# Kernel optimization log

Measured on AMD Instinct MI355X. Metric: run time of the kernel, lower is better.

Reference implementation:

```python
import jax, jax.numpy as jnp
import numpy as np
from jax import lax

B, D_MODEL, H, W = 8, 384, 64, 64
D_INNER, D_STATE, D_CONV, DT_RANK = 768, 16, 4, 24
C3, MLP_H = 3 * D_MODEL, 4 * D_MODEL
EPS = 1e-5


def setup_inputs():
    key = jax.random.key(0)
    ks = jax.random.split(key, 16)
    r = lambda i, shape, s=0.02: jax.random.normal(ks[i], shape, jnp.float32) * s
    return {
        'x': jax.random.normal(ks[0], (B, D_MODEL, H, W), jnp.float32),
        'ln1_g': jnp.ones((D_MODEL,), jnp.float32), 'ln1_b': jnp.zeros((D_MODEL,), jnp.float32),
        'in_w': r(1, (2 * D_INNER, D_MODEL)),
        'conv_w': r(2, (D_INNER, 1, D_CONV), 0.2), 'conv_b': jnp.zeros((D_INNER,), jnp.float32),
        'xproj_w': r(3, (DT_RANK + 2 * D_STATE, D_INNER)),
        'dtproj_w': r(4, (D_INNER, DT_RANK), 0.1),
        'dtproj_b': jnp.full((D_INNER,), jnp.log(jnp.expm1(0.01)).item(), jnp.float32),
        'A_log': jnp.log(jnp.broadcast_to(jnp.arange(1, D_STATE + 1, dtype=jnp.float32), (D_INNER, D_STATE))),
        'Dskip': jnp.ones((D_INNER,), jnp.float32),
        'out_w': r(5, (D_MODEL, D_INNER)),
        'dw_w': r(6, (C3, 1, 3, 3), 0.1),
        'bn_g': jnp.ones((C3,), jnp.float32), 'bn_b': jnp.zeros((C3,), jnp.float32),
        'bn_mean': jnp.zeros((C3,), jnp.float32), 'bn_var': jnp.ones((C3,), jnp.float32),
        'pw_w': r(7, (C3, C3)),
        'fus_w': r(8, (D_MODEL, D_MODEL)), 'fus_b': jnp.zeros((D_MODEL,), jnp.float32),
        'ln2_g': jnp.ones((D_MODEL,), jnp.float32), 'ln2_b': jnp.zeros((D_MODEL,), jnp.float32),
        'mlp_w1': r(9, (MLP_H, D_MODEL)), 'mlp_b1': jnp.zeros((MLP_H,), jnp.float32),
        'mlp_w2': r(10, (D_MODEL, MLP_H)), 'mlp_b2': jnp.zeros((D_MODEL,), jnp.float32),
    }


def _ln(x, g, b):
    m = x.mean(-1, keepdims=True)
    v = ((x - m) ** 2).mean(-1, keepdims=True)
    return (x - m) / jnp.sqrt(v + EPS) * g + b


def _dwt(x):
    x01 = x[:, :, 0::2, :] / 2
    x02 = x[:, :, 1::2, :] / 2
    x1, x3 = x01[:, :, :, 0::2], x01[:, :, :, 1::2]
    x2, x4 = x02[:, :, :, 0::2], x02[:, :, :, 1::2]
    ll = x1 + x2 + x3 + x4
    hl = -x1 - x2 + x3 + x4
    lh = -x1 + x2 - x3 + x4
    hh = x1 - x2 - x3 + x4
    return ll, jnp.concatenate([hl, lh, hh], axis=1)


def _idwt(ll, high):
    b, c, h, w = ll.shape
    hl, lh, hh = jnp.split(high, 3, axis=1)
    h_ll, h_hl, h_lh, h_hh = ll / 2, hl / 2, lh / 2, hh / 2
    y1 = h_ll - h_hl - h_lh + h_hh  # (even row, even col)
    y2 = h_ll - h_hl + h_lh - h_hh  # (odd row, even col)
    y3 = h_ll + h_hl - h_lh - h_hh  # (even row, odd col)
    y4 = h_ll + h_hl + h_lh + h_hh  # (odd row, odd col)
    row_e = jnp.stack([y1, y3], axis=-1).reshape(b, c, h, 2 * w)
    row_o = jnp.stack([y2, y4], axis=-1).reshape(b, c, h, 2 * w)
    return jnp.stack([row_e, row_o], axis=-2).reshape(b, c, 2 * h, 2 * w)


def _mamba(x, in_w, conv_w, conv_b, xproj_w, dtproj_w, dtproj_b, A_log, Dskip, out_w):
    # x: [B, L, d_model]
    bb = x.shape[0]
    xz = x @ in_w.T  # [B,L,2*d_inner]
    xi, z = jnp.split(xz, 2, axis=-1)
    xc = jnp.swapaxes(xi, 1, 2)  # [B,d_inner,L]
    xc = lax.conv_general_dilated(xc, conv_w, (1,), [(D_CONV - 1, 0)],
                                  feature_group_count=D_INNER,
                                  dimension_numbers=('NCH', 'OIH', 'NCH')) + conv_b[None, :, None]
    u = jax.nn.silu(jnp.swapaxes(xc, 1, 2))  # [B,L,d_inner]
    dbl = u @ xproj_w.T
    dtr = dbl[..., :DT_RANK]
    Bm = dbl[..., DT_RANK:DT_RANK + D_STATE]
    Cm = dbl[..., DT_RANK + D_STATE:]
    dt = jax.nn.softplus(dtr @ dtproj_w.T + dtproj_b)  # [B,L,d_inner]
    A = -jnp.exp(A_log)  # [d_inner,d_state]

    def step(h, t):
        dt_t, B_t, C_t, u_t = t
        dA = jnp.exp(dt_t[:, :, None] * A)
        h = dA * h + (dt_t * u_t)[:, :, None] * B_t[:, None, :]
        return h, jnp.sum(h * C_t[:, None, :], axis=-1)

    h0 = jnp.zeros((bb, D_INNER, D_STATE), x.dtype)
    xs = (jnp.swapaxes(dt, 0, 1), jnp.swapaxes(Bm, 0, 1), jnp.swapaxes(Cm, 0, 1), jnp.swapaxes(u, 0, 1))
    _, ys = lax.scan(step, h0, xs)
    y = jnp.swapaxes(ys, 0, 1) + u * Dskip
    y = y * jax.nn.silu(z)
    return y @ out_w.T


def reference(x, ln1_g, ln1_b, in_w, conv_w, conv_b, xproj_w, dtproj_w, dtproj_b,
              A_log, Dskip, out_w, dw_w, bn_g, bn_b, bn_mean, bn_var, pw_w,
              fus_w, fus_b, ln2_g, ln2_b, mlp_w1, mlp_b1, mlp_w2, mlp_b2):
    shortcut = x
    x_ll, x_high = _dwt(x)
    b, c, hh, ww = x_ll.shape
    # LL branch: LN -> Mamba -> residual
    x_ll_in = _ln(jnp.transpose(x_ll, (0, 2, 3, 1)), ln1_g, ln1_b)
    y = _mamba(x_ll_in.reshape(b, hh * ww, c), in_w, conv_w, conv_b, xproj_w,
               dtproj_w, dtproj_b, A_log, Dskip, out_w)
    x_ll_out = x_ll + jnp.transpose(y.reshape(b, hh, ww, c), (0, 3, 1, 2))
    # High-freq branch: depthwise3x3 -> BN(eval) -> SiLU -> 1x1 -> residual
    hd = lax.conv_general_dilated(x_high, dw_w, (1, 1), [(1, 1), (1, 1)],
                                  feature_group_count=C3,
                                  dimension_numbers=('NCHW', 'OIHW', 'NCHW'))
    hd = (hd - bn_mean[None, :, None, None]) / jnp.sqrt(bn_var + EPS)[None, :, None, None] \
         * bn_g[None, :, None, None] + bn_b[None, :, None, None]
    hd = jax.nn.silu(hd)
    x_high_out = x_high + jnp.einsum('bchw,oc->bohw', hd, pw_w)
    # Reconstruct + fusion 1x1 conv + residual
    recon = _idwt(x_ll_out, x_high_out)
    recon = jnp.einsum('bchw,oc->bohw', recon, fus_w) + fus_b[None, :, None, None]
    x2 = shortcut + recon
    # LN + MLP + residual
    xn = _ln(jnp.transpose(x2, (0, 2, 3, 1)), ln2_g, ln2_b)
    m = jax.nn.gelu(xn @ mlp_w1.T + mlp_b1, approximate=False) @ mlp_w2.T + mlp_b2
    return x2 + jnp.transpose(m, (0, 3, 1, 2))
```

## Files before the change

### kernel.cpp

```cpp
#include <hip/hip_runtime.h>
#include <hip/hip_bf16.h>
#include <math.h>

typedef __hip_bfloat16 bf16;
typedef __attribute__((ext_vector_type(8))) short bf16x8;
typedef __attribute__((ext_vector_type(4))) float f32x4;
typedef unsigned short u16;

#define LN_EPS 1e-5f

__device__ inline u16 f2b(float v) {
    __hip_bfloat16 h = __float2bfloat16(v);
    return *reinterpret_cast<u16*>(&h);
}

__device__ inline float b2f_lo(unsigned int w) { return __uint_as_float(w << 16); }
__device__ inline float b2f_hi(unsigned int w) { return __uint_as_float(w & 0xFFFF0000u); }

__device__ inline void gload_lds16(const void* g, void* l) {
    __builtin_amdgcn_global_load_lds(
        (const __attribute__((address_space(1))) void*)(uintptr_t)g,
        (__attribute__((address_space(3))) void*)(uintptr_t)(unsigned int)(uintptr_t)l,
        16, 0, 0);
}
__device__ inline void gload_lds4(const void* g, void* l) {
    __builtin_amdgcn_global_load_lds(
        (const __attribute__((address_space(1))) void*)(uintptr_t)g,
        (__attribute__((address_space(3))) void*)(uintptr_t)(unsigned int)(uintptr_t)l,
        4, 0, 0);
}

__global__ __launch_bounds__(256) void sentinel_kernel(float* __restrict__ out, int n) {
    int i = blockIdx.x * 256 + threadIdx.x;
    if (i < n) out[i] = 123.0f;
}

__global__ __launch_bounds__(256) void reduce12_kernel(const float* __restrict__ P,
                                                       float* __restrict__ out, int n4) {
    int i = blockIdx.x * 256 + threadIdx.x;
    if (i >= n4) return;
    const float4* p4 = (const float4*)P;
    float4 s = p4[i];
#pragma unroll
    for (int z = 1; z < 12; z++) {
        float4 v = p4[(size_t)z * n4 + i];
        s.x += v.x; s.y += v.y; s.z += v.z; s.w += v.w;
    }
    ((float4*)out)[i] = s;
}

__global__ void detect_kernel(const unsigned int* __restrict__ g, int* __restrict__ flag) {
    *flag = (*g == 0x3F803F80u) ? 1 : 0;
}

struct Jobs {
    const void* src[25];
    int prefix[26];
};
__global__ __launch_bounds__(256) void convert_kernel(Jobs J, u16* __restrict__ dst16,
                                                      float* __restrict__ dst32,
                                                      const int* __restrict__ flag) {
    int i = blockIdx.x * 256 + threadIdx.x;
    int total = J.prefix[25];
    if (i >= total) return;
    int f = *flag;
    int lo = 0;
    while (J.prefix[lo + 1] <= i) lo++;
    int off = i - J.prefix[lo];
    float v = f ? (float)((const bf16*)J.src[lo])[off] : ((const float*)J.src[lo])[off];
    if (lo < 6) dst16[i] = f2b(v);
    else        dst32[i - J.prefix[6]] = v;
}

__global__ __launch_bounds__(256) void dwt_kernel(const void* __restrict__ xv,
                                                  float* __restrict__ xll,
                                                  float* __restrict__ xhigh,
                                                  const int* __restrict__ flag) {
    __shared__ float tile[32][133];
    int blk = blockIdx.x;
    int cc = blk % 12;
    int t2 = blk / 12;
    int i  = t2 % 32;
    int b  = t2 / 32;
    int t  = threadIdx.x;
    int c_l = t >> 3;
    int sub = t & 7;
    size_t rowbase = ((size_t)(b * 384 + cc * 32 + c_l)) * 4096 + (size_t)i * 128;
    if (*flag) {
        const u16* xp = (const u16*)xv + rowbase;
#pragma unroll
        for (int k = 0; k < 2; k++) {
            int e0 = (sub + k * 8) * 8;
            uint4 v = *(const uint4*)(xp + e0);
            tile[c_l][e0 + 0] = b2f_lo(v.x); tile[c_l][e0 + 1] = b2f_hi(v.x);
            tile[c_l][e0 + 2] = b2f_lo(v.y); tile[c_l][e0 + 3] = b2f_hi(v.y);
            tile[c_l][e0 + 4] = b2f_lo(v.z); tile[c_l][e0 + 5] = b2f_hi(v.z);
            tile[c_l][e0 + 6] = b2f_lo(v.w); tile[c_l][e0 + 7] = b2f_hi(v.w);
        }
    } else {
        const float* xp = (const float*)xv + rowbase;
#pragma unroll
        for (int k = 0; k < 4; k++) {
            int f0 = (sub + k * 8) * 4;
            float4 v = *(const float4*)(xp + f0);
            tile[c_l][f0 + 0] = v.x; tile[c_l][f0 + 1] = v.y;
            tile[c_l][f0 + 2] = v.z; tile[c_l][f0 + 3] = v.w;
        }
    }
    __syncthreads();
    int c_out = t & 31;
    int jg = t >> 5;
    int cg = cc * 32 + c_out;
#pragma unroll
    for (int jj = 0; jj < 4; jj++) {
        int j = jg * 4 + jj;
        float A = tile[c_out][2 * j];
        float B = tile[c_out][2 * j + 1];
        float C = tile[c_out][64 + 2 * j];
        float D = tile[c_out][64 + 2 * j + 1];
        float ll = 0.5f * (A + B + C + D);
        float hl = 0.5f * (B + D - A - C);
        float lh = 0.5f * (C + D - A - B);
        float hh = 0.5f * (A + D - B - C);
        int pm = b * 1024 + i * 32 + j;
        xll[(size_t)pm * 384 + cg] = ll;
        size_t hb = (size_t)pm * 1152;
        xhigh[hb + cg] = hl;
        xhigh[hb + 384 + cg] = lh;
        xhigh[hb + 768 + cg] = hh;
    }
}

template <bool OBF>
__global__ __launch_bounds__(128) void ln_kernel(const float* __restrict__ in,
                                                 void* __restrict__ outv,
                                                 const float* __restrict__ g,
                                                 const float* __restrict__ b) {
    const int C = 384;
    int row = blockIdx.x;
    int t = threadIdx.x;
    const float* rp = in + (size_t)row * C;
    float v0 = rp[t], v1 = rp[t + 128], v2 = rp[t + 256];
    __shared__ float red[128];
    red[t] = v0 + v1 + v2;
    __syncthreads();
    for (int off = 64; off > 0; off >>= 1) {
        if (t < off) red[t] += red[t + off];
        __syncthreads();
    }
    float mean = red[0] * (1.f / 384.f);
    __syncthreads();
    float d0 = v0 - mean, d1 = v1 - mean, d2 = v2 - mean;
    red[t] = d0 * d0 + d1 * d1 + d2 * d2;
    __syncthreads();
    for (int off = 64; off > 0; off >>= 1) {
        if (t < off) red[t] += red[t + off];
        __syncthreads();
    }
    float inv = rsqrtf(red[0] * (1.f / 384.f) + LN_EPS);
    float o0 = d0 * inv * g[t]       + b[t];
    float o1 = d1 * inv * g[t + 128] + b[t + 128];
    float o2 = d2 * inv * g[t + 256] + b[t + 256];
    if constexpr (OBF) {
        u16* op = (u16*)outv + (size_t)row * C;
        op[t] = f2b(o0); op[t + 128] = f2b(o1); op[t + 256] = f2b(o2);
    } else {
        float* op = (float*)outv + (size_t)row * C;
        op[t] = o0; op[t + 128] = o1; op[t + 256] = o2;
    }
}

#define EP_NONE 0
#define EP_SOFTPLUS_BIAS 1
#define EP_ADD 2
#define EP_FUS 3
#define EP_GELU_BIAS 4
#define EP_FINAL 5

template <int EPIL, bool CBF>
__global__ __launch_bounds__(256) void gemm_mfma(const u16* __restrict__ A, int lda,
                                                 const u16* __restrict__ W,
                                                 void* __restrict__ Cp, int ldc,
                                                 int M, int N, int K,
                                                 const float* __restrict__ addsrc,
                                                 const float* __restrict__ bias,
                                                 const void* __restrict__ xres,
                                                 void* __restrict__ obf,
                                                 int m_off,
                                                 const int* __restrict__ flag) {
    __shared__ u16 Als[3][128][32];
    __shared__ u16 Bls[3][128][32];
    const int t = threadIdx.x;
    const int wave = t >> 6, lane = t & 63;
    const int quad = lane >> 4, r16 = lane & 15;
    const int wm = (wave >> 1) * 64, wn = (wave & 1) * 64;
    const int mb = blockIdx.x * 128, nb = blockIdx.y * 128;
    f32x4 acc[4][4] = {};

    const int srow = wave * 32 + (lane >> 2);
    const int scol = (lane & 3) * 8;
    const u16* Ag0 = A + (size_t)(mb + srow) * lda + scol;
    const u16* Ag1 = A + (size_t)(mb + srow + 16) * lda + scol;
    const u16* Wg0 = W + (size_t)(nb + srow) * (size_t)K + scol;
    const u16* Wg1 = W + (size_t)(nb + srow + 16) * (size_t)K + scol;

    auto stage = [&](int buf, int kt) {
        int k0 = kt * 32;
        gload_lds16(Ag0 + k0, &Als[buf][wave * 32][0]);
        gload_lds16(Ag1 + k0, &Als[buf][wave * 32 + 16][0]);
        gload_lds16(Wg0 + k0, &Bls[buf][wave * 32][0]);
        gload_lds16(Wg1 + k0, &Bls[buf][wave * 32 + 16][0]);
    };

    const int NK = K >> 5;
    stage(0, 0);
    if (NK > 1) stage(1, 1);

    for (int kt = 0; kt < NK; kt++) {
        if (kt + 1 < NK) asm volatile("s_waitcnt vmcnt(4)" ::: "memory");
        else             asm volatile("s_waitcnt vmcnt(0)" ::: "memory");
        __builtin_amdgcn_s_barrier();
        asm volatile("" ::: "memory");
        int pf = kt + 2;
        if (pf < NK) stage(pf % 3, pf);
        const int cb = kt % 3;
        bf16x8 af[4], bfv[4];
#pragma unroll
        for (int i = 0; i < 4; i++) af[i] = *(const bf16x8*)&Als[cb][wm + i * 16 + r16][quad * 8];
#pragma unroll
        for (int j = 0; j < 4; j++) bfv[j] = *(const bf16x8*)&Bls[cb][wn + j * 16 + r16][quad * 8];
#pragma unroll
        for (int i = 0; i < 4; i++)
#pragma unroll
            for (int j = 0; j < 4; j++)
                acc[i][j] = __builtin_amdgcn_mfma_f32_16x16x32_bf16(af[i], bfv[j], acc[i][j], 0, 0, 0);
    }

    int f = 0;
    if constexpr (EPIL == EP_FUS || EPIL == EP_FINAL) f = *flag;
#pragma unroll
    for (int i = 0; i < 4; i++) {
#pragma unroll
        for (int j = 0; j < 4; j++) {
#pragma unroll
            for (int rg = 0; rg < 4; rg++) {
                int m = mb + wm + i * 16 + quad * 4 + rg;
                int n = nb + wn + j * 16 + r16;
                float v = acc[i][j][rg];
                if constexpr (EPIL == EP_NONE) {
                    if constexpr (CBF) ((u16*)Cp)[(size_t)m * ldc + n] = f2b(v);
                    else               ((float*)Cp)[(size_t)m * ldc + n] = v;
                } else if constexpr (EPIL == EP_ADD) {
                    ((float*)Cp)[(size_t)m * ldc + n] = addsrc[(size_t)m * ldc + n] + v;
                } else if constexpr (EPIL == EP_FUS) {
                    v += bias[n];
                    int bb = m >> 12, pix = m & 4095;
                    size_t xi = ((size_t)(bb * 384 + n) << 12) + pix;
                    v += f ? (float)((const bf16*)xres)[xi] : ((const float*)xres)[xi];
                    ((float*)Cp)[(size_t)m * ldc + n] = v;
                } else if constexpr (EPIL == EP_GELU_BIAS) {
                    v += bias[n];
                    v = 0.5f * v * (1.f + erff(v * 0.70710678118654752f));
                    if constexpr (CBF) ((u16*)Cp)[(size_t)m * ldc + n] = f2b(v);
                    else               ((float*)Cp)[(size_t)m * ldc + n] = v;
                } else if constexpr (EPIL == EP_FINAL) {
                    v += bias[n];
                    int gm = m_off + m;
                    v += addsrc[(size_t)gm * 384 + n];
                    int bb = gm >> 12, pix = gm & 4095;
                    size_t oi = ((size_t)(bb * 384 + n) << 12) + pix;
                    if (f) ((bf16*)obf)[oi] = __float2bfloat16(v);
                    else   ((float*)obf)[oi] = v;
                }
            }
        }
    }
}

template <int EPIL, bool SPLITK>
__global__ __launch_bounds__(256) void gemm_nt(const float* __restrict__ A, int lda,
                                               const float* __restrict__ W,
                                               float* __restrict__ C, int ldc,
                                               int M, int N, int K,
                                               const float* __restrict__ bias,
                                               int kc) {
    __shared__ __align__(16) float As[16][68];
    __shared__ __align__(16) float Bs[16][68];
    int t = threadIdx.x;
    int mb = blockIdx.y * 64;
    int nb = blockIdx.x * 64;
    int kb = SPLITK ? blockIdx.z * kc : 0;
    int ke = SPLITK ? kb + kc : K;
    int tm = t & 15, tn = t >> 4;
    float* Cout = C;
    if constexpr (SPLITK) Cout = C + (size_t)blockIdx.z * (size_t)M * ldc;
    float acc[4][4] = {};
    for (int k0 = kb; k0 < ke; k0 += 16) {
#pragma unroll
        for (int i = 0; i < 4; i++) {
            int idx = t + i * 256;
            int r = idx >> 4, c = idx & 15;
            float v = 0.f;
            if (k0 + c < K) v = A[(size_t)(mb + r) * lda + k0 + c];
            As[c][r] = v;
        }
#pragma unroll
        for (int i = 0; i < 4; i++) {
            int idx = t + i * 256;
            int r = idx >> 4, c = idx & 15;
            float v = 0.f;
            if ((nb + r) < N && (k0 + c) < K) v = W[(size_t)(nb + r) * K + k0 + c];
            Bs[c][r] = v;
        }
        __syncthreads();
#pragma unroll
        for (int kk = 0; kk < 16; kk++) {
            float4 av = *(const float4*)&As[kk][tm * 4];
            float4 bv = *(const float4*)&Bs[kk][tn * 4];
            float a4[4] = {av.x, av.y, av.z, av.w};
            float b4[4] = {bv.x, bv.y, bv.z, bv.w};
#pragma unroll
            for (int i = 0; i < 4; i++)
#pragma unroll
                for (int j = 0; j < 4; j++) acc[i][j] += a4[i] * b4[j];
        }
        __syncthreads();
    }
#pragma unroll
    for (int i = 0; i < 4; i++) {
        int m = mb + tm * 4 + i;
        if (m >= M) continue;
#pragma unroll
        for (int j = 0; j < 4; j++) {
            int n = nb + tn * 4 + j;
            if (n >= N) continue;
            float v = acc[i][j];
            if constexpr (SPLITK) {
                Cout[(size_t)m * ldc + n] = v;
            } else if constexpr (EPIL == EP_NONE) {
                C[(size_t)m * ldc + n] = v;
            } else if constexpr (EPIL == EP_SOFTPLUS_BIAS) {
                v += bias[n];
                v = (v > 20.f) ? v : log1pf(expf(v));
                C[(size_t)m * ldc + n] = v;
            }
        }
    }
}

__global__ __launch_bounds__(256) void conv1d_silu_kernel(const float* __restrict__ xz,
                                                          const float* __restrict__ cw,
                                                          const float* __restrict__ cb,
                                                          float* __restrict__ u) {
    int tid = blockIdx.x * 256 + threadIdx.x;
    int dq = tid % 192;
    int t2 = tid / 192;
    int l = t2 % 1024;
    int b = t2 / 1024;
    int d = dq * 4;
    float4 q0 = *(const float4*)&cw[d * 4];
    float4 q1 = *(const float4*)&cw[d * 4 + 4];
    float4 q2 = *(const float4*)&cw[d * 4 + 8];
    float4 q3 = *(const float4*)&cw[d * 4 + 12];
    float4 acc = *(const float4*)&cb[d];
    int rowbase = b * 1024;
#pragma unroll
    for (int k = 0; k < 4; k++) {
        int ls = l - 3 + k;
        if (ls < 0) continue;
        float4 xv = *(const float4*)&xz[(size_t)(rowbase + ls) * 1536 + d];
        acc.x += ((const float*)&q0)[k] * xv.x;
        acc.y += ((const float*)&q1)[k] * xv.y;
        acc.z += ((const float*)&q2)[k] * xv.z;
        acc.w += ((const float*)&q3)[k] * xv.w;
    }
    float4 o;
    o.x = acc.x / (1.f + __expf(-acc.x));
    o.y = acc.y / (1.f + __expf(-acc.y));
    o.z = acc.z / (1.f + __expf(-acc.z));
    o.w = acc.w / (1.f + __expf(-acc.w));
    *(float4*)&u[(size_t)(rowbase + l) * 768 + d] = o;
}

__device__ inline void scan_load_ac(const float* __restrict__ A_log, int d,
                                    float (&Ac)[16], bool& structured) {
#pragma unroll
    for (int s = 0; s < 16; s++) Ac[s] = -__expf(A_log[d * 16 + s]);
    structured = true;
#pragma unroll
    for (int s = 0; s < 16; s++)
        structured = structured && (fabsf(Ac[s] - (s + 1) * Ac[0]) <= 1e-5f * fabsf(Ac[s]));
}

__global__ __launch_bounds__(256) void scan_p1(const float* __restrict__ dt,
                                               const float* __restrict__ u,
                                               const float* __restrict__ dbl,
                                               const float* __restrict__ A_log,
                                               float* __restrict__ st) {
    __shared__ float Bsh[2][16][16];
    int tloc = threadIdx.x;
    int idx = blockIdx.x * 256 + tloc;
    int p = idx >> 1;
    int sh = idx & 1;
    int g = p % 6144;
    int c = p / 6144;
    int d = g % 768, b = g / 768;
    float Ac[16]; bool structured;
    scan_load_ac(A_log, d, Ac, structured);
    int s0 = sh * 8;
    float h[8];
#pragma unroll
    for (int s = 0; s < 8; s++) h[s] = 0.f;
    float S = 0.f;
    size_t m0 = (size_t)b * 1024 + c * 128;
    const int jj = tloc >> 4, ff = tloc & 15;
    float* lbase0 = &Bsh[0][0][0] + (tloc >> 6) * 64;
    float* lbase1 = &Bsh[1][0][0] + (tloc >> 6) * 64;
    gload_lds4(&dbl[(m0 + jj) * 56 + 24 + ff], lbase0);
    __syncthreads();
    for (int grp = 0; grp < 8; grp++) {
        int cur = grp & 1;
        if (grp + 1 < 8) {
            gload_lds4(&dbl[(m0 + (grp + 1) * 16 + jj) * 56 + 24 + ff],
                       cur ? lbase0 : lbase1);
        }
        float dtb[16], ub[16];
#pragma unroll
        for (int j = 0; j < 16; j++) {
            size_t m = m0 + grp * 16 + j;
            dtb[j] = dt[m * 768 + d];
            ub[j]  = u[m * 768 + d];
        }
        if (structured) {
#pragma unroll
            for (int j = 0; j < 16; j++) {
                float dtv = dtb[j];
                float du = dtv * ub[j];
                S += dtv;
                float q  = __expf(dtv * Ac[0]);
                float q2 = q * q, q3 = q2 * q, q4 = q2 * q2;
                float q5 = q4 * q, q6 = q4 * q2, q7 = q4 * q3, q8 = q4 * q4;
                float base = sh ? q8 : 1.f;
                float a[8] = {base * q,  base * q2, base * q3, base * q4,
                              base * q5, base * q6, base * q7, base * q8};
#pragma unroll
                for (int s = 0; s < 8; s++)
                    h[s] = a[s] * h[s] + du * Bsh[cur][j][s0 + s];
            }
        } else {
#pragma unroll
            for (int j = 0; j < 16; j++) {
                float dtv = dtb[j];
                float du = dtv * ub[j];
                S += dtv;
#pragma unroll
                for (int s = 0; s < 8; s++)
                    h[s] = __expf(dtv * Ac[s0 + s]) * h[s] + du * Bsh[cur][j][s0 + s];
            }
        }
        __syncthreads();
    }
    float* stp = st + (size_t)(c * 6144 + g) * 32;
#pragma unroll
    for (int s = 0; s < 8; s++) stp[s0 + s] = __expf(Ac[s0 + s] * S);
#pragma unroll
    for (int s = 0; s < 8; s++) stp[16 + s0 + s] = h[s];
}

__global__ __launch_bounds__(256) void scan_p2(float* __restrict__ st) {
    int tid = blockIdx.x * 256 + threadIdx.x;
    int s = tid & 15;
    int g = tid >> 4;
    float H = 0.f;
#pragma unroll
    for (int c = 0; c < 8; c++) {
        size_t i = (size_t)(c * 6144 + g) * 32;
        float P  = st[i + s];
        float hE = st[i + 16 + s];
        st[i + s] = H;
        H = hE + P * H;
    }
}

__global__ __launch_bounds__(256) void scan_p3(const float* __restrict__ dt,
                                               const float* __restrict__ u,
                                               const float* __restrict__ dbl,
                                               const float* __restrict__ z,
                                               const float* __restrict__ A_log,
                                               const float* __restrict__ Dskip,
                                               const float* __restrict__ st,
                                               u16* __restrict__ ybuf) {
    __shared__ float BCsh[2][8][32];
    int tloc = threadIdx.x;
    int idx = blockIdx.x * 256 + tloc;
    int p = idx >> 1;
    int sh = idx & 1;
    int g = p % 6144;
    int c = p / 6144;
    int d = g % 768, b = g / 768;
    float Ac[16]; bool structured;
    scan_load_ac(A_log, d, Ac, structured);
    int s0 = sh * 8;
    float Dsk = Dskip[d];
    float h[8];
    const float* stp = st + (size_t)(c * 6144 + g) * 32;
#pragma unroll
    for (int s = 0; s < 8; s++) h[s] = stp[s0 + s];
    size_t m0 = (size_t)b * 1024 + c * 128;
    const int jj = tloc >> 5, ff = tloc & 31;
    float* lbase0 = &BCsh[0][0][0] + (tloc >> 6) * 64;
    float* lbase1 = &BCsh[1][0][0] + (tloc >> 6) * 64;
    gload_lds4(&dbl[(m0 + jj) * 56 + 24 + ff], lbase0);
    __syncthreads();
    for (int grp = 0; grp < 16; grp++) {
        int cur = grp & 1;
        if (grp + 1 < 16) {
            gload_lds4(&dbl[(m0 + (grp + 1) * 8 + jj) * 56 + 24 + ff],
                       cur ? lbase0 : lbase1);
        }
        float dtb[8], ub[8], zb[8];
#pragma unroll
        for (int j = 0; j < 8; j++) {
            size_t m = m0 + grp * 8 + j;
            dtb[j] = dt[m * 768 + d];
            ub[j]  = u[m * 768 + d];
            zb[j]  = z[m * 1536 + 768 + d];
        }
#pragma unroll
        for (int j = 0; j < 8; j++) {
            size_t m = m0 + grp * 8 + j;
            float dtv = dtb[j];
            float uv  = ub[j];
            float zv  = zb[j];
            float du = dtv * uv;
            if (structured) {
                float q  = __expf(dtv * Ac[0]);
                float q2 = q * q, q3 = q2 * q, q4 = q2 * q2;
                float q5 = q4 * q, q6 = q4 * q2, q7 = q4 * q3, q8 = q4 * q4;
                float base = sh ? q8 : 1.f;
                float a[8] = {base * q,  base * q2, base * q3, base * q4,
                              base * q5, base * q6, base * q7, base * q8};
#pragma unroll
                for (int s = 0; s < 8; s++)
                    h[s] = a[s] * h[s] + du * BCsh[cur][j][s0 + s];
            } else {
#pragma unroll
                for (int s = 0; s < 8; s++)
                    h[s] = __expf(dtv * Ac[s0 + s]) * h[s] + du * BCsh[cur][j][s0 + s];
            }
            float pr[8];
#pragma unroll
            for (int s = 0; s < 8; s++) pr[s] = h[s] * BCsh[cur][j][16 + s0 + s];
            float y = ((pr[0] + pr[1]) + (pr[2] + pr[3])) + ((pr[4] + pr[5]) + (pr[6] + pr[7]));
            y += __shfl_xor(y, 1);
            if (!sh) {
                float sig = 1.f / (1.f + __expf(-zv));
                ybuf[m * 3072 + d] = f2b((y + uv * Dsk) * (zv * sig));
            }
        }
        __syncthreads();
    }
}

__global__ __launch_bounds__(256) void dwconv_bn_silu_kernel(const float* __restrict__ xh,
                                                             const float* __restrict__ w,
                                                             const float* __restrict__ g,
                                                             const float* __restrict__ bb,
                                                             const float* __restrict__ mean,
                                                             const float* __restrict__ var,
                                                             u16* __restrict__ hd) {
    int tid = blockIdx.x * 256 + threadIdx.x;
    int cq = tid % 288;
    int t2 = tid / 288;
    int xc = t2 & 3;
    int t3 = t2 >> 2;
    int y = t3 % 32;
    int b = t3 / 32;
    int c = cq * 4;
    float wk[9][4];
#pragma unroll
    for (int i = 0; i < 4; i++) {
        float4 wa = *(const float4*)&w[(c + i) * 9];
        float4 wbv = *(const float4*)&w[(c + i) * 9 + 4];
        float wcv = w[(c + i) * 9 + 8];
        wk[0][i] = wa.x; wk[1][i] = wa.y; wk[2][i] = wa.z; wk[3][i] = wa.w;
        wk[4][i] = wbv.x; wk[5][i] = wbv.y; wk[6][i] = wbv.z; wk[7][i] = wbv.w;
        wk[8][i] = wcv;
    }
    float4 mn = *(const float4*)&mean[c];
    float4 vr = *(const float4*)&var[c];
    float4 gg = *(const float4*)&g[c];
    float4 bv = *(const float4*)&bb[c];
    float scl[4], sft[4];
    scl[0] = rsqrtf(vr.x + LN_EPS) * gg.x; sft[0] = bv.x - mn.x * scl[0];
    scl[1] = rsqrtf(vr.y + LN_EPS) * gg.y; sft[1] = bv.y - mn.y * scl[1];
    scl[2] = rsqrtf(vr.z + LN_EPS) * gg.z; sft[2] = bv.z - mn.z * scl[2];
    scl[3] = rsqrtf(vr.w + LN_EPS) * gg.w; sft[3] = bv.w - mn.w * scl[3];

    int x0 = xc * 8;
    size_t pixbase = (size_t)b * 1024 + y * 32;
    float win[3][3][4];
    auto ldcol = [&](int xx, float (&col)[3][4]) {
#pragma unroll
        for (int r = 0; r < 3; r++) {
            int yy = y + r - 1;
            if (xx < 0 || xx > 31 || yy < 0 || yy > 31) {
                col[r][0] = col[r][1] = col[r][2] = col[r][3] = 0.f;
            } else {
                float4 v = *(const float4*)&xh[((size_t)b * 1024 + yy * 32 + xx) * 1152 + c];
                col[r][0] = v.x; col[r][1] = v.y; col[r][2] = v.z; col[r][3] = v.w;
            }
        }
    };
    ldcol(x0 - 1, win[0]);
    ldcol(x0, win[1]);
#pragma unroll
    for (int xi = 0; xi < 8; xi++) {
        int x = x0 + xi;
        ldcol(x + 1, win[2]);
        ushort4 o;
        u16* op = (u16*)&o;
#pragma unroll
        for (int i = 0; i < 4; i++) {
            float acc = 0.f;
#pragma unroll
            for (int ky = 0; ky < 3; ky++)
#pragma unroll
                for (int kx = 0; kx < 3; kx++)
                    acc += wk[ky * 3 + kx][i] * win[kx][ky][i];
            float vv = acc * scl[i] + sft[i];
            op[i] = f2b(vv / (1.f + __expf(-vv)));
        }
        *(ushort4*)&hd[(pixbase + x) * 1152 + c] = o;
#pragma unroll
        for (int r = 0; r < 3; r++)
#pragma unroll
            for (int i = 0; i < 4; i++) {
                win[0][r][i] = win[1][r][i];
                win[1][r][i] = win[2][r][i];
            }
    }
}

__global__ __launch_bounds__(256) void idwt_kernel(const float* __restrict__ xll,
                                                   const float* __restrict__ xh,
                                                   u16* __restrict__ recon) {
    int idx = blockIdx.x * 256 + threadIdx.x;
    int c = idx % 384;
    int t = idx / 384;
    int p = t % 1024;
    int b = t / 1024;
    int i = p >> 5, j = p & 31;
    float ll = xll[(size_t)(b * 1024 + p) * 384 + c];
    int hb = (b * 1024 + p) * 1152;
    float hl = xh[hb + c];
    float lh = xh[hb + 384 + c];
    float hh = xh[hb + 768 + c];
    float y1 = 0.5f * (ll - hl - lh + hh);
    float y3 = 0.5f * (ll + hl - lh - hh);
    float y2 = 0.5f * (ll - hl + lh - hh);
    float y4 = 0.5f * (ll + hl + lh + hh);
    int r0 = b * 4096 + (2 * i) * 64 + 2 * j;
    recon[(size_t)r0 * 384 + c] = f2b(y1);
    recon[(size_t)(r0 + 1) * 384 + c] = f2b(y3);
    recon[(size_t)(r0 + 64) * 384 + c] = f2b(y2);
    recon[(size_t)(r0 + 65) * 384 + c] = f2b(y4);
}

extern "C" void kernel_launch(void* const* d_in, const int* in_sizes, int n_in,
                              void* d_out, int out_size, void* d_ws, size_t ws_size,
                              hipStream_t stream) {
    const void* x = d_in[0];
    void* out = d_out;

    float* ws = (float*)d_ws;
    float* x_ll    = ws;
    float* x_high  = ws + 3145728;
    u16*   mlp_hid = (u16*)ws;
    float* xz      = ws + 12582912;
    u16*   ybuf    = (u16*)xz;
    u16*   hd      = (u16*)xz;
    u16*   recon   = (u16*)(ws + 17301504);
    u16*   xn      = recon;
    float* u       = ws + 25165824;
    float* dt      = ws + 31457280;
    u16*   x_ll_in = (u16*)dt;
    float* xpart   = dt;
    float* x2      = ws + 25165824;
    float* dbl     = ws + 37748736;
    float* scanst  = ws + 38207488;

    u16* wb16 = (u16*)(ws + 39780352);
    u16* b_in_w   = wb16;
    u16* b_out_w  = wb16 + 589824;
    u16* b_pw_w   = wb16 + 884736;
    u16* b_fus_w  = wb16 + 2211840;
    u16* b_mlp_w1 = wb16 + 2359296;
    u16* b_mlp_w2 = wb16 + 2949120;
    float* f32base = ws + 39780352 + 1769472;
    float* c_conv_w   = f32base;
    float* c_conv_b   = f32base + 3072;
    float* c_xproj_w  = f32base + 3840;
    float* c_dtproj_w = f32base + 46848;
    float* c_dtproj_b = f32base + 65280;
    float* c_A_log    = f32base + 66048;
    float* c_Dskip    = f32base + 78336;
    float* c_dw_w     = f32base + 79104;
    float* c_bn_g     = f32base + 89472;
    float* c_bn_b     = f32base + 90624;
    float* c_bn_mean  = f32base + 91776;
    float* c_bn_var   = f32base + 92928;
    float* c_ln1_g    = f32base + 94080;
    float* c_ln1_b    = f32base + 94464;
    float* c_ln2_g    = f32base + 94848;
    float* c_ln2_b    = f32base + 95232;
    float* c_fus_b    = f32base + 95616;
    float* c_mlp_b1   = f32base + 96000;
    float* c_mlp_b2   = f32base + 97536;
    int* flag = (int*)(f32base + 97920);

    if (ws_size < (size_t)(39780352 + 1769472 + 97920 + 2) * 4) {
        sentinel_kernel<<<(out_size + 255) / 256, 256, 0, stream>>>((float*)out, out_size);
        return;
    }

    detect_kernel<<<1, 1, 0, stream>>>((const unsigned int*)d_in[1], flag);
    Jobs J;
    const int src_idx[25] = {3, 11, 17, 18, 22, 24,
                             4, 5, 6, 7, 8, 9, 10, 12, 13, 14, 15, 16,
                             1, 2, 20, 21, 19, 23, 25};
    const int joff[26] = {0, 589824, 884736, 2211840, 2359296, 2949120, 3538944,
                          3538944 + 3072, 3538944 + 3840, 3538944 + 46848, 3538944 + 65280,
                          3538944 + 66048, 3538944 + 78336, 3538944 + 79104, 3538944 + 89472,
                          3538944 + 90624, 3538944 + 91776, 3538944 + 92928, 3538944 + 94080,
                          3538944 + 94464, 3538944 + 94848, 3538944 + 95232, 3538944 + 95616,
                          3538944 + 96000, 3538944 + 97536, 3538944 + 97920};
    for (int i = 0; i < 25; i++) J.src[i] = d_in[src_idx[i]];
    for (int i = 0; i < 26; i++) J.prefix[i] = joff[i];
    convert_kernel<<<(3636864 + 255) / 256, 256, 0, stream>>>(J, wb16, f32base, flag);

    dwt_kernel<<<3072, 256, 0, stream>>>(x, x_ll, x_high, flag);
    ln_kernel<true><<<8192, 128, 0, stream>>>(x_ll, x_ll_in, c_ln1_g, c_ln1_b);
    gemm_mfma<EP_NONE, false><<<dim3(64, 12), 256, 0, stream>>>(x_ll_in, 384, b_in_w, xz, 1536,
                                                                8192, 1536, 384, nullptr, nullptr, nullptr, nullptr, 0, flag);
    conv1d_silu_kernel<<<6144, 256, 0, stream>>>(xz, c_conv_w, c_conv_b, u);
    gemm_nt<EP_NONE, true><<<dim3(1, 128, 12), 256, 0, stream>>>(u, 768, c_xproj_w, xpart, 56,
                                                                 8192, 56, 768, nullptr, 64);
    reduce12_kernel<<<(114688 + 255) / 256, 256, 0, stream>>>(xpart, dbl, 114688);
    gemm_nt<EP_SOFTPLUS_BIAS, false><<<dim3(12, 128), 256, 0, stream>>>(dbl, 56, c_dtproj_w, dt, 768,
                                                                        8192, 768, 24, c_dtproj_b, 0);
    scan_p1<<<384, 256, 0, stream>>>(dt, u, dbl, c_A_log, scanst);
    scan_p2<<<384, 256, 0, stream>>>(scanst);
    scan_p3<<<384, 256, 0, stream>>>(dt, u, dbl, xz, c_A_log, c_Dskip, scanst, ybuf);
    gemm_mfma<EP_ADD, false><<<dim3(64, 3), 256, 0, stream>>>(ybuf, 3072, b_out_w, x_ll, 384,
                                                              8192, 384, 768, x_ll, nullptr, nullptr, nullptr, 0, flag);
    dwconv_bn_silu_kernel<<<1152, 256, 0, stream>>>(x_high, c_dw_w, c_bn_g, c_bn_b, c_bn_mean, c_bn_var, hd);
    gemm_mfma<EP_ADD, false><<<dim3(64, 9), 256, 0, stream>>>(hd, 1152, b_pw_w, x_high, 1152,
                                                              8192, 1152, 1152, x_high, nullptr, nullptr, nullptr, 0, flag);
    idwt_kernel<<<12288, 256, 0, stream>>>(x_ll, x_high, recon);
    gemm_mfma<EP_FUS, false><<<dim3(256, 3), 256, 0, stream>>>(recon, 384, b_fus_w, x2, 384,
                                                               32768, 384, 384, nullptr, c_fus_b, x, nullptr, 0, flag);
    ln_kernel<true><<<32768, 128, 0, stream>>>(x2, xn, c_ln2_g, c_ln2_b);
    for (int ck = 0; ck < 2; ck++) {
        const u16* xn_c = xn + (size_t)ck * 16384 * 384;
        gemm_mfma<EP_GELU_BIAS, true><<<dim3(128, 12), 256, 0, stream>>>(xn_c, 384, b_mlp_w1, mlp_hid, 1536,
                                                                         16384, 1536, 384, nullptr, c_mlp_b1, nullptr, nullptr, 0, flag);
        gemm_mfma<EP_FINAL, false><<<dim3(128, 3), 256, 0, stream>>>(mlp_hid, 1536, b_mlp_w2, nullptr, 0,
                                                                     16384, 384, 1536, x2, c_mlp_b2, nullptr, out, ck * 16384, flag);
    }
}
```

Measured before the change: 692.8 us.

## Fuse dt projection and softplus into scan kernels, drop dt GEMM

Removes the separate dt-projection GEMM that wrote an 8192x768 dt buffer. Both scan_p1 and scan_p3 now hold the 24-wide dtproj_w row per channel in registers. They stage the first 24 columns of dbl in LDS alongside B/C and compute softplus(w·x + b) inline. This saves one kernel launch and the dt write plus two reads, at the price of recomputing the 24-term dot product and log1p/exp in both scan passes and higher register and LDS use.

```diff
diff --git a/kernel.cpp b/kernel.cpp
--- a/kernel.cpp
+++ b/kernel.cpp
@@ -392,12 +392,14 @@
         structured = structured && (fabsf(Ac[s] - (s + 1) * Ac[0]) <= 1e-5f * fabsf(Ac[s]));
 }
 
-__global__ __launch_bounds__(256) void scan_p1(const float* __restrict__ dt,
-                                               const float* __restrict__ u,
+__global__ __launch_bounds__(256) void scan_p1(const float* __restrict__ u,
                                                const float* __restrict__ dbl,
                                                const float* __restrict__ A_log,
+                                               const float* __restrict__ wproj,
+                                               const float* __restrict__ wbias,
                                                float* __restrict__ st) {
     __shared__ float Bsh[2][16][16];
+    __shared__ float Dsh[2][16][32];
     int tloc = threadIdx.x;
     int idx = blockIdx.x * 256 + tloc;
     int p = idx >> 1;
@@ -408,6 +410,10 @@
     float Ac[16]; bool structured;
     scan_load_ac(A_log, d, Ac, structured);
     int s0 = sh * 8;
+    float wrow[24];
+#pragma unroll
+    for (int k = 0; k < 24; k++) wrow[k] = wproj[d * 24 + k];
+    float bd = wbias[d];
     float h[8];
 #pragma unroll
     for (int s = 0; s < 8; s++) h[s] = 0.f;
@@ -416,27 +422,36 @@
     const int jj = tloc >> 4, ff = tloc & 15;
     float* lbase0 = &Bsh[0][0][0] + (tloc >> 6) * 64;
     float* lbase1 = &Bsh[1][0][0] + (tloc >> 6) * 64;
+    const int dr1 = tloc >> 5,        ds1c = (tloc & 31) < 24 ? (tloc & 31) : 23;
+    const int dr2 = (256 + tloc) >> 5, ds2c = (tloc & 31) < 24 ? (tloc & 31) : 23;
+    float* dA0 = &Dsh[0][0][0] + (tloc >> 6) * 64;
+    float* dB0 = &Dsh[0][0][0] + 256 + (tloc >> 6) * 64;
+    float* dA1 = &Dsh[1][0][0] + (tloc >> 6) * 64;
+    float* dB1 = &Dsh[1][0][0] + 256 + (tloc >> 6) * 64;
     gload_lds4(&dbl[(m0 + jj) * 56 + 24 + ff], lbase0);
+    gload_lds4(&dbl[(m0 + dr1) * 56 + ds1c], dA0);
+    gload_lds4(&dbl[(m0 + dr2) * 56 + ds2c], dB0);
     __syncthreads();
     for (int grp = 0; grp < 8; grp++) {
         int cur = grp & 1;
         if (grp + 1 < 8) {
-            gload_lds4(&dbl[(m0 + (grp + 1) * 16 + jj) * 56 + 24 + ff],
-                       cur ? lbase0 : lbase1);
-        }
-        float dtb[16], ub[16];
+            size_t mn = m0 + (size_t)(grp + 1) * 16;
+            gload_lds4(&dbl[(mn + jj) * 56 + 24 + ff], cur ? lbase0 : lbase1);
+            gload_lds4(&dbl[(mn + dr1) * 56 + ds1c], cur ? dA0 : dA1);
+            gload_lds4(&dbl[(mn + dr2) * 56 + ds2c], cur ? dB0 : dB1);
+        }
+        float ub[16];
+#pragma unroll
+        for (int j = 0; j < 16; j++) ub[j] = u[(m0 + grp * 16 + j) * 768 + d];
 #pragma unroll
         for (int j = 0; j < 16; j++) {
-            size_t m = m0 + grp * 16 + j;
-            dtb[j] = dt[m * 768 + d];
-            ub[j]  = u[m * 768 + d];
-        }
-        if (structured) {
-#pragma unroll
-            for (int j = 0; j < 16; j++) {
-                float dtv = dtb[j];
-                float du = dtv * ub[j];
-                S += dtv;
+            float xx = bd;
+#pragma unroll
+            for (int k = 0; k < 24; k++) xx += wrow[k] * Dsh[cur][j][k];
+            float dtv = (xx > 20.f) ? xx : log1pf(expf(xx));
+            float du = dtv * ub[j];
+            S += dtv;
+            if (structured) {
                 float q  = __expf(dtv * Ac[0]);
                 float q2 = q * q, q3 = q2 * q, q4 = q2 * q2;
                 float q5 = q4 * q, q6 = q4 * q2, q7 = q4 * q3, q8 = q4 * q4;
@@ -446,13 +461,7 @@
 #pragma unroll
                 for (int s = 0; s < 8; s++)
                     h[s] = a[s] * h[s] + du * Bsh[cur][j][s0 + s];
-            }
-        } else {
-#pragma unroll
-            for (int j = 0; j < 16; j++) {
-                float dtv = dtb[j];
-                float du = dtv * ub[j];
-                S += dtv;
+            } else {
 #pragma unroll
                 for (int s = 0; s < 8; s++)
                     h[s] = __expf(dtv * Ac[s0 + s]) * h[s] + du * Bsh[cur][j][s0 + s];
@@ -482,15 +491,17 @@
     }
 }
 
-__global__ __launch_bounds__(256) void scan_p3(const float* __restrict__ dt,
-                                               const float* __restrict__ u,
+__global__ __launch_bounds__(256) void scan_p3(const float* __restrict__ u,
                                                const float* __restrict__ dbl,
                                                const float* __restrict__ z,
                                                const float* __restrict__ A_log,
+                                               const float* __restrict__ wproj,
+                                               const float* __restrict__ wbias,
                                                const float* __restrict__ Dskip,
                                                const float* __restrict__ st,
                                                u16* __restrict__ ybuf) {
     __shared__ float BCsh[2][8][32];
+    __shared__ float Dsh[2][8][32];
     int tloc = threadIdx.x;
     int idx = blockIdx.x * 256 + tloc;
     int p = idx >> 1;
@@ -501,6 +512,10 @@
     float Ac[16]; bool structured;
     scan_load_ac(A_log, d, Ac, structured);
     int s0 = sh * 8;
+    float wrow[24];
+#pragma unroll
+    for (int k = 0; k < 24; k++) wrow[k] = wproj[d * 24 + k];
+    float bd = wbias[d];
     float Dsk = Dskip[d];
     float h[8];
     const float* stp = st + (size_t)(c * 6144 + g) * 32;
@@ -510,26 +525,33 @@
     const int jj = tloc >> 5, ff = tloc & 31;
     float* lbase0 = &BCsh[0][0][0] + (tloc >> 6) * 64;
     float* lbase1 = &BCsh[1][0][0] + (tloc >> 6) * 64;
+    const int dslotc = (tloc & 31) < 24 ? (tloc & 31) : 23;
+    float* dA0 = &Dsh[0][0][0] + (tloc >> 6) * 64;
+    float* dA1 = &Dsh[1][0][0] + (tloc >> 6) * 64;
     gload_lds4(&dbl[(m0 + jj) * 56 + 24 + ff], lbase0);
+    gload_lds4(&dbl[(m0 + jj) * 56 + dslotc], dA0);
     __syncthreads();
     for (int grp = 0; grp < 16; grp++) {
         int cur = grp & 1;
         if (grp + 1 < 16) {
-            gload_lds4(&dbl[(m0 + (grp + 1) * 8 + jj) * 56 + 24 + ff],
-                       cur ? lbase0 : lbase1);
-        }
-        float dtb[8], ub[8], zb[8];
+            size_t mn = m0 + (size_t)(grp + 1) * 8;
+            gload_lds4(&dbl[(mn + jj) * 56 + 24 + ff], cur ? lbase0 : lbase1);
+            gload_lds4(&dbl[(mn + jj) * 56 + dslotc], cur ? dA0 : dA1);
+        }
+        float ub[8], zb[8];
 #pragma unroll
         for (int j = 0; j < 8; j++) {
             size_t m = m0 + grp * 8 + j;
-            dtb[j] = dt[m * 768 + d];
-            ub[j]  = u[m * 768 + d];
-            zb[j]  = z[m * 1536 + 768 + d];
+            ub[j] = u[m * 768 + d];
+            zb[j] = z[m * 1536 + 768 + d];
         }
 #pragma unroll
         for (int j = 0; j < 8; j++) {
             size_t m = m0 + grp * 8 + j;
-            float dtv = dtb[j];
+            float xx = bd;
+#pragma unroll
+            for (int k = 0; k < 24; k++) xx += wrow[k] * Dsh[cur][j][k];
+            float dtv = (xx > 20.f) ? xx : log1pf(expf(xx));
             float uv  = ub[j];
             float zv  = zb[j];
             float du = dtv * uv;
@@ -747,11 +769,9 @@
     gemm_nt<EP_NONE, true><<<dim3(1, 128, 12), 256, 0, stream>>>(u, 768, c_xproj_w, xpart, 56,
                                                                  8192, 56, 768, nullptr, 64);
     reduce12_kernel<<<(114688 + 255) / 256, 256, 0, stream>>>(xpart, dbl, 114688);
-    gemm_nt<EP_SOFTPLUS_BIAS, false><<<dim3(12, 128), 256, 0, stream>>>(dbl, 56, c_dtproj_w, dt, 768,
-                                                                        8192, 768, 24, c_dtproj_b, 0);
-    scan_p1<<<384, 256, 0, stream>>>(dt, u, dbl, c_A_log, scanst);
+    scan_p1<<<384, 256, 0, stream>>>(u, dbl, c_A_log, c_dtproj_w, c_dtproj_b, scanst);
     scan_p2<<<384, 256, 0, stream>>>(scanst);
-    scan_p3<<<384, 256, 0, stream>>>(dt, u, dbl, xz, c_A_log, c_Dskip, scanst, ybuf);
+    scan_p3<<<384, 256, 0, stream>>>(u, dbl, xz, c_A_log, c_dtproj_w, c_dtproj_b, c_Dskip, scanst, ybuf);
     gemm_mfma<EP_ADD, false><<<dim3(64, 3), 256, 0, stream>>>(ybuf, 3072, b_out_w, x_ll, 384,
                                                               8192, 384, 768, x_ll, nullptr, nullptr, nullptr, 0, flag);
     dwconv_bn_silu_kernel<<<1152, 256, 0, stream>>>(x_high, c_dw_w, c_bn_g, c_bn_b, c_bn_mean, c_bn_var, hd);
```

New measurement: 787.3 us. 13.6% more time.
